# Kernel tuning notes

Hardware: AMD Instinct MI355X
Metric: run time of the kernel (lower is better)

Reference implementation:

```python
import jax, jax.numpy as jnp
import numpy as np

B, N, F = 4096, 64, 128   # batch, max_neighbor, input feature dim
H, D = 8, 64              # num_heads, weight_dims (per head)
HD = H * D


def setup_inputs() -> dict:
    key = jax.random.key(0)
    k1, k2, k3, k4 = jax.random.split(key, 4)
    x = jax.random.normal(k1, (B, N, F), dtype=jnp.float32)
    W_lin = jax.random.normal(k2, (F, HD), dtype=jnp.float32) * (1.0 / np.sqrt(F))
    W_att = jax.random.normal(k3, (2 * HD, H), dtype=jnp.float32) * (1.0 / np.sqrt(2 * HD))
    mask = jax.random.randint(k4, (B, N), 0, 2, dtype=jnp.int32)
    return {"x": x, "W_lin": W_lin, "W_att": W_att, "mask": mask}


def reference(x, W_lin, W_att, mask):
    # dropout is identity (rate 0.0 / inference)
    lin = x @ W_lin                               # [B, N, H*D]
    # src node is neighbor slot 0 of each batch row (the Python-loop gather+tile)
    src = lin[:, 0, :]                            # [B, H*D]
    # attention_layer on concat([src, lin]) == src@W_att[:HD] + lin@W_att[HD:]
    att = src @ W_att[:HD]                        # [B, H]
    att = att[:, None, :] + lin @ W_att[HD:]      # [B, N, H]
    att = jnp.where(att >= 0, att, 0.2 * att)     # LeakyReLU(alpha=0.2)
    aw = jnp.transpose(att, (0, 2, 1))            # [B, H, N]  (split heads + squeeze)
    aw = aw + (mask == 0).astype(jnp.float32)[:, None, :] * (-1e9)
    aw = jax.nn.softmax(aw, axis=2)[..., None]    # [B, H, N, 1]
    lp = jnp.transpose(lin.reshape(B, N, H, D), (0, 2, 1, 3))  # [B, H, N, D]
    weighted = lp * aw                            # [B, H, N, D]
    # fusion 'concat': unstack heads, concat along last -> [B, N, H*D], then ReLU
    out = jnp.transpose(weighted, (0, 2, 1, 3)).reshape(B, N, HD)
    return jax.nn.relu(out)
```

## Files before the change

kernel.cpp:

```cpp
#include <hip/hip_runtime.h>


typedef _Float16 half8 __attribute__((ext_vector_type(8)));
typedef _Float16 half4v __attribute__((ext_vector_type(4)));
typedef float f32x4 __attribute__((ext_vector_type(4)));

static constexpr int NSEQ = 64;
static constexpr int FIN  = 128;
static constexpr int HDIM = 512;
static constexpr int NHEAD = 8;
static constexpr int LIN_LD = 520;
static constexpr int XS_LD  = 136;

__global__ __launch_bounds__(256) void prep_kernel(const float* __restrict__ wlin,
                                                   const float* __restrict__ watt,
                                                   _Float16* __restrict__ wlinT,
                                                   _Float16* __restrict__ wacat)
{
    int t = blockIdx.x * 256 + threadIdx.x;
    if (t < HDIM * FIN) {
        int c = t >> 7;
        int k = t & 127;
        wlinT[t] = (_Float16)wlin[k * HDIM + c];
    }
    if (t < 16 * HDIM) {
        int col = t >> 9;
        int k = t & 511;
        float v = (col < NHEAD) ? watt[(HDIM + k) * NHEAD + col]
                                : watt[k * NHEAD + (col - NHEAD)];
        wacat[t] = (_Float16)v;
    }
}

__global__ __launch_bounds__(256, 2) void fused_kernel(const float* __restrict__ x,
                                                       const _Float16* __restrict__ wlinT,
                                                       const _Float16* __restrict__ wacat,
                                                       const int* __restrict__ mask,
                                                       float* __restrict__ out)
{
    __shared__ _Float16 lin_s[NSEQ * LIN_LD];
    __shared__ float attbuf[NSEQ * 17];
    __shared__ float aw_s[NSEQ * NHEAD];

    const int b    = blockIdx.x;
    const int t    = threadIdx.x;
    const int lane = t & 63;
    const int w    = t >> 6;
    const int l15  = lane & 15;
    const int quad = lane >> 4;

    _Float16* xs = lin_s;

    const float4* xb = (const float4*)(x + (size_t)b * (NSEQ * FIN));
    #pragma unroll
    for (int it = 0; it < 8; ++it) {
        int i = it * 256 + t;
        float4 v = xb[i];
        int n = i >> 5;
        int k = (i & 31) << 2;
        half4v hv;
        hv[0] = (_Float16)v.x; hv[1] = (_Float16)v.y;
        hv[2] = (_Float16)v.z; hv[3] = (_Float16)v.w;
        *(half4v*)(xs + n * XS_LD + k) = hv;
    }
    __syncthreads();

    f32x4 acc[4][8];
    #pragma unroll
    for (int mt = 0; mt < 4; ++mt)
        #pragma unroll
        for (int nt = 0; nt < 8; ++nt)
            acc[mt][nt] = (f32x4){0.f, 0.f, 0.f, 0.f};

    const int colbase = w * 128;
    #pragma unroll
    for (int ks = 0; ks < 4; ++ks) {
        const int k0 = ks * 32 + quad * 8;
        half8 bf[8];
        #pragma unroll
        for (int nt = 0; nt < 8; ++nt) {
            int col = colbase + nt * 16 + l15;
            bf[nt] = *(const half8*)(wlinT + col * FIN + k0);
        }
        #pragma unroll
        for (int mt = 0; mt < 4; ++mt) {
            half8 af = *(const half8*)(xs + (mt * 16 + l15) * XS_LD + k0);
            #pragma unroll
            for (int nt = 0; nt < 8; ++nt)
                acc[mt][nt] = __builtin_amdgcn_mfma_f32_16x16x32_f16(af, bf[nt], acc[mt][nt], 0, 0, 0);
        }
    }
    __syncthreads();

    #pragma unroll
    for (int mt = 0; mt < 4; ++mt)
        #pragma unroll
        for (int nt = 0; nt < 8; ++nt)
            #pragma unroll
            for (int i = 0; i < 4; ++i) {
                int row = mt * 16 + quad * 4 + i;
                int col = colbase + nt * 16 + l15;
                lin_s[row * LIN_LD + col] = (_Float16)acc[mt][nt][i];
            }
    __syncthreads();

    f32x4 acca = (f32x4){0.f, 0.f, 0.f, 0.f};
    #pragma unroll
    for (int ks = 0; ks < 16; ++ks) {
        int k0 = ks * 32 + quad * 8;
        half8 af = *(const half8*)(lin_s + (w * 16 + l15) * LIN_LD + k0);
        half8 bf = *(const half8*)(wacat + l15 * HDIM + k0);
        acca = __builtin_amdgcn_mfma_f32_16x16x32_f16(af, bf, acca, 0, 0, 0);
    }
    #pragma unroll
    for (int i = 0; i < 4; ++i)
        attbuf[(w * 16 + quad * 4 + i) * 17 + l15] = acca[i];
    __syncthreads();

    const int mv = mask[b * NSEQ + lane];
    const float pen = (mv == 0) ? -1e9f : 0.0f;
    #pragma unroll
    for (int rep = 0; rep < 2; ++rep) {
        int hh = w + rep * 4;
        float srcv = attbuf[8 + hh];
        float a = attbuf[lane * 17 + hh] + srcv;
        a = (a >= 0.0f) ? a : 0.2f * a;
        a += pen;
        float mx = a;
        #pragma unroll
        for (int off = 32; off > 0; off >>= 1)
            mx = fmaxf(mx, __shfl_xor(mx, off, 64));
        float e = __expf(a - mx);
        float s = e;
        #pragma unroll
        for (int off = 32; off > 0; off >>= 1)
            s += __shfl_xor(s, off, 64);
        aw_s[lane * NHEAD + hh] = e / s;
    }
    __syncthreads();

    float4* ob = (float4*)(out + (size_t)b * (NSEQ * HDIM));
    #pragma unroll
    for (int it = 0; it < 32; ++it) {
        int i = it * 256 + t;
        int n = i >> 7;
        int c = (i & 127) << 2;
        float wgt = aw_s[n * NHEAD + (c >> 6)];
        half4v lv = *(const half4v*)(lin_s + n * LIN_LD + c);
        float4 o;
        o.x = fmaxf((float)lv[0] * wgt, 0.0f);
        o.y = fmaxf((float)lv[1] * wgt, 0.0f);
        o.z = fmaxf((float)lv[2] * wgt, 0.0f);
        o.w = fmaxf((float)lv[3] * wgt, 0.0f);
        ob[i] = o;
    }
}

extern "C" void kernel_launch(void* const* d_in, const int* in_sizes, int n_in,
                              void* d_out, int out_size, void* d_ws, size_t ws_size,
                              hipStream_t stream)
{
    const float* x    = (const float*)d_in[0];
    const float* wlin = (const float*)d_in[1];
    const float* watt = (const float*)d_in[2];
    const int*   mask = (const int*)d_in[3];
    float* out = (float*)d_out;

    _Float16* wlinT = (_Float16*)d_ws;
    _Float16* wacat = wlinT + HDIM * FIN;

    const int B = in_sizes[0] / (NSEQ * FIN);

    prep_kernel<<<256, 256, 0, stream>>>(wlin, watt, wlinT, wacat);
    fused_kernel<<<B, 256, 0, stream>>>(x, wlinT, wacat, mask, out);
}
```

Measured before the change: 666.5 us.

## Use 512-thread blocks with swapped MFMA operands and nontemporal global I/O

Doubles the block to 8 waves, so each wave computes a 64-column slice of the projection. The MFMA operand roles are swapped so each lane's accumulator holds consecutive columns, which allows packed half4 stores into shared memory. The attention-score GEMM is split over K across two wave groups whose partial results are summed, and each wave now handles one head's softmax. Global loads of x and stores of the output use nontemporal hints to cut cache pollution on this streaming, bandwidth-bound kernel, at the cost of more shared memory for the attention buffer and a tighter register budget.

```diff
diff --git a/kernel.cpp b/kernel.cpp
--- a/kernel.cpp
+++ b/kernel.cpp
@@ -5,9 +5,9 @@
 typedef _Float16 half4v __attribute__((ext_vector_type(4)));
 typedef float f32x4 __attribute__((ext_vector_type(4)));
 
-static constexpr int NSEQ = 64;
-static constexpr int FIN  = 128;
-static constexpr int HDIM = 512;
+static constexpr int NSEQ  = 64;
+static constexpr int FIN   = 128;
+static constexpr int HDIM  = 512;
 static constexpr int NHEAD = 8;
 static constexpr int LIN_LD = 520;
 static constexpr int XS_LD  = 136;
@@ -32,14 +32,14 @@
     }
 }
 
-__global__ __launch_bounds__(256, 2) void fused_kernel(const float* __restrict__ x,
+__global__ __launch_bounds__(512, 4) void fused_kernel(const float* __restrict__ x,
                                                        const _Float16* __restrict__ wlinT,
                                                        const _Float16* __restrict__ wacat,
                                                        const int* __restrict__ mask,
                                                        float* __restrict__ out)
 {
     __shared__ _Float16 lin_s[NSEQ * LIN_LD];
-    __shared__ float attbuf[NSEQ * 17];
+    __shared__ float attbuf[2 * NSEQ * 17];
     __shared__ float aw_s[NSEQ * NHEAD];
 
     const int b    = blockIdx.x;
@@ -51,43 +51,41 @@
 
     _Float16* xs = lin_s;
 
-    const float4* xb = (const float4*)(x + (size_t)b * (NSEQ * FIN));
+    const f32x4* xb = (const f32x4*)(x + (size_t)b * (NSEQ * FIN));
     #pragma unroll
-    for (int it = 0; it < 8; ++it) {
-        int i = it * 256 + t;
-        float4 v = xb[i];
+    for (int it = 0; it < 4; ++it) {
+        int i = it * 512 + t;
+        f32x4 v = __builtin_nontemporal_load(&xb[i]);
         int n = i >> 5;
         int k = (i & 31) << 2;
         half4v hv;
-        hv[0] = (_Float16)v.x; hv[1] = (_Float16)v.y;
-        hv[2] = (_Float16)v.z; hv[3] = (_Float16)v.w;
+        hv[0] = (_Float16)v[0]; hv[1] = (_Float16)v[1];
+        hv[2] = (_Float16)v[2]; hv[3] = (_Float16)v[3];
         *(half4v*)(xs + n * XS_LD + k) = hv;
     }
     __syncthreads();
 
-    f32x4 acc[4][8];
+    f32x4 acc[4][4];
     #pragma unroll
     for (int mt = 0; mt < 4; ++mt)
         #pragma unroll
-        for (int nt = 0; nt < 8; ++nt)
+        for (int nt = 0; nt < 4; ++nt)
             acc[mt][nt] = (f32x4){0.f, 0.f, 0.f, 0.f};
 
-    const int colbase = w * 128;
+    const int colbase = w * 64;
     #pragma unroll
     for (int ks = 0; ks < 4; ++ks) {
         const int k0 = ks * 32 + quad * 8;
-        half8 bf[8];
+        half8 a[4];
         #pragma unroll
-        for (int nt = 0; nt < 8; ++nt) {
-            int col = colbase + nt * 16 + l15;
-            bf[nt] = *(const half8*)(wlinT + col * FIN + k0);
-        }
+        for (int mt = 0; mt < 4; ++mt)
+            a[mt] = *(const half8*)(wlinT + (colbase + mt * 16 + l15) * FIN + k0);
         #pragma unroll
-        for (int mt = 0; mt < 4; ++mt) {
-            half8 af = *(const half8*)(xs + (mt * 16 + l15) * XS_LD + k0);
+        for (int nt = 0; nt < 4; ++nt) {
+            half8 bfr = *(const half8*)(xs + (nt * 16 + l15) * XS_LD + k0);
             #pragma unroll
-            for (int nt = 0; nt < 8; ++nt)
-                acc[mt][nt] = __builtin_amdgcn_mfma_f32_16x16x32_f16(af, bf[nt], acc[mt][nt], 0, 0, 0);
+            for (int mt = 0; mt < 4; ++mt)
+                acc[mt][nt] = __builtin_amdgcn_mfma_f32_16x16x32_f16(a[mt], bfr, acc[mt][nt], 0, 0, 0);
         }
     }
     __syncthreads();
@@ -95,35 +93,37 @@
     #pragma unroll
     for (int mt = 0; mt < 4; ++mt)
         #pragma unroll
-        for (int nt = 0; nt < 8; ++nt)
+        for (int nt = 0; nt < 4; ++nt) {
+            half4v hv;
             #pragma unroll
-            for (int i = 0; i < 4; ++i) {
-                int row = mt * 16 + quad * 4 + i;
-                int col = colbase + nt * 16 + l15;
-                lin_s[row * LIN_LD + col] = (_Float16)acc[mt][nt][i];
-            }
+            for (int i = 0; i < 4; ++i) hv[i] = (_Float16)acc[mt][nt][i];
+            *(half4v*)(lin_s + (nt * 16 + l15) * LIN_LD + colbase + mt * 16 + quad * 4) = hv;
+        }
     __syncthreads();
 
-    f32x4 acca = (f32x4){0.f, 0.f, 0.f, 0.f};
-    #pragma unroll
-    for (int ks = 0; ks < 16; ++ks) {
-        int k0 = ks * 32 + quad * 8;
-        half8 af = *(const half8*)(lin_s + (w * 16 + l15) * LIN_LD + k0);
-        half8 bf = *(const half8*)(wacat + l15 * HDIM + k0);
-        acca = __builtin_amdgcn_mfma_f32_16x16x32_f16(af, bf, acca, 0, 0, 0);
+    {
+        const int rt = w & 3;
+        const int kh = w >> 2;
+        f32x4 acca = (f32x4){0.f, 0.f, 0.f, 0.f};
+        #pragma unroll
+        for (int ks = 0; ks < 8; ++ks) {
+            int k0 = kh * 256 + ks * 32 + quad * 8;
+            half8 af = *(const half8*)(lin_s + (rt * 16 + l15) * LIN_LD + k0);
+            half8 bf = *(const half8*)(wacat + l15 * HDIM + k0);
+            acca = __builtin_amdgcn_mfma_f32_16x16x32_f16(af, bf, acca, 0, 0, 0);
+        }
+        #pragma unroll
+        for (int i = 0; i < 4; ++i)
+            attbuf[kh * NSEQ * 17 + (rt * 16 + quad * 4 + i) * 17 + l15] = acca[i];
     }
-    #pragma unroll
-    for (int i = 0; i < 4; ++i)
-        attbuf[(w * 16 + quad * 4 + i) * 17 + l15] = acca[i];
     __syncthreads();
 
-    const int mv = mask[b * NSEQ + lane];
-    const float pen = (mv == 0) ? -1e9f : 0.0f;
-    #pragma unroll
-    for (int rep = 0; rep < 2; ++rep) {
-        int hh = w + rep * 4;
-        float srcv = attbuf[8 + hh];
-        float a = attbuf[lane * 17 + hh] + srcv;
+    {
+        const int mv = mask[b * NSEQ + lane];
+        const float pen = (mv == 0) ? -1e9f : 0.0f;
+        const int h = w;
+        float srcv = attbuf[8 + h] + attbuf[NSEQ * 17 + 8 + h];
+        float a = attbuf[lane * 17 + h] + attbuf[NSEQ * 17 + lane * 17 + h] + srcv;
         a = (a >= 0.0f) ? a : 0.2f * a;
         a += pen;
         float mx = a;
@@ -135,24 +135,24 @@
         #pragma unroll
         for (int off = 32; off > 0; off >>= 1)
             s += __shfl_xor(s, off, 64);
-        aw_s[lane * NHEAD + hh] = e / s;
+        aw_s[lane * NHEAD + h] = e / s;
     }
     __syncthreads();
 
-    float4* ob = (float4*)(out + (size_t)b * (NSEQ * HDIM));
+    f32x4* ob = (f32x4*)(out + (size_t)b * (NSEQ * HDIM));
     #pragma unroll
-    for (int it = 0; it < 32; ++it) {
-        int i = it * 256 + t;
+    for (int it = 0; it < 16; ++it) {
+        int i = it * 512 + t;
         int n = i >> 7;
         int c = (i & 127) << 2;
         float wgt = aw_s[n * NHEAD + (c >> 6)];
         half4v lv = *(const half4v*)(lin_s + n * LIN_LD + c);
-        float4 o;
-        o.x = fmaxf((float)lv[0] * wgt, 0.0f);
-        o.y = fmaxf((float)lv[1] * wgt, 0.0f);
-        o.z = fmaxf((float)lv[2] * wgt, 0.0f);
-        o.w = fmaxf((float)lv[3] * wgt, 0.0f);
-        ob[i] = o;
+        f32x4 o;
+        o[0] = fmaxf((float)lv[0] * wgt, 0.0f);
+        o[1] = fmaxf((float)lv[1] * wgt, 0.0f);
+        o[2] = fmaxf((float)lv[2] * wgt, 0.0f);
+        o[3] = fmaxf((float)lv[3] * wgt, 0.0f);
+        __builtin_nontemporal_store(o, &ob[i]);
     }
 }
 
@@ -172,5 +172,5 @@
     const int B = in_sizes[0] / (NSEQ * FIN);
 
     prep_kernel<<<256, 256, 0, stream>>>(wlin, watt, wlinT, wacat);
-    fused_kernel<<<B, 256, 0, stream>>>(x, wlinT, wacat, mask, out);
+    fused_kernel<<<B, 512, 0, stream>>>(x, wlinT, wacat, mask, out);
 }
```

New measurement: 648.0 us. 1.03x faster.
